# Performance work log

Hardware: AMD Instinct MI355X
Metric: run time of the kernel (lower is better)

Reference implementation:

```python
import jax, jax.numpy as jnp
import numpy as np

R = 5            # num_relations
NEG_SLOPE = 0.2
N1 = 30000       # layer0 target count
N2 = 15000       # layer1 target count


def brgcn_conv(x_src, x_tgt, edge_index, edge_type, Wj, Wi, att_j, att_i,
               Wq, Wk, Wv, sw, sb, Wrel, heads, outc):
    """One BRGCNConv layer: per-relation GAT edge softmax + bilevel relation attention."""
    N = x_tgt.shape[0]
    hc = heads * outc
    hj = (x_src @ Wj).reshape(-1, heads, outc)   # [Ns,H,C]
    hi = (x_tgt @ Wi).reshape(-1, heads, outc)   # [N,H,C]
    src, tgt = edge_index[0], edge_index[1]
    xj = hj[src]                                  # [E,H,C]
    xi = hi[tgt]                                  # [E,H,C]
    # relation-specific attention logits per edge
    aj = jnp.sum(att_j[edge_type] * xj, axis=-1)  # [E,H]
    ai = jnp.sum(att_i[edge_type] * xi, axis=-1)  # [E,H]
    alpha = jax.nn.leaky_relu(aj + ai, NEG_SLOPE)
    # edge softmax grouped by (target node, relation) == per-relation propagate
    seg = tgt * R + edge_type                     # [E]
    nseg = N * R
    amax = jax.ops.segment_max(alpha, seg, num_segments=nseg)
    amax = jnp.where(jnp.isfinite(amax), amax, 0.0)
    ex = jnp.exp(alpha - amax[seg])
    den = jax.ops.segment_sum(ex, seg, num_segments=nseg)
    w = ex / jnp.maximum(den[seg], 1e-16)         # [E,H]
    msg = (w[:, :, None] * xj).reshape(-1, hc)    # [E,H*C]
    z = jax.ops.segment_sum(msg, seg, num_segments=nseg)
    z = z.reshape(N, R, hc).transpose(1, 0, 2)    # [R,N,H*C]; zero rows where no edges
    # per-relation Q/K/V
    q = jnp.einsum('rnd,rde->rne', z, Wq).reshape(R, N, heads, outc)
    k = jnp.einsum('rnd,rde->rne', z, Wk).reshape(R, N, heads, outc)
    v = jnp.einsum('rnd,rde->rne', z, Wv).reshape(R, N, heads, outc)
    # bilevel relation attention: psi[r,s,n,h] = <q_r, k_s>
    psi = jnp.einsum('rnhc,snhc->rsnh', q, k)
    mask = (psi == 0) & (jnp.sum(psi, axis=1, keepdims=True) != 0)
    prob = jax.nn.softmax(jnp.where(mask, -jnp.inf, psi), axis=1)
    delta = jnp.einsum('rsnh,snhc->rnhc', prob, v).reshape(R, N, hc)
    out = jnp.einsum('rnd,r->nd', delta, Wrel[:, 0])
    # single node type -> node_self[0] applied to every target node
    return out + x_tgt @ sw + sb


def setup_inputs() -> dict:
    key = jax.random.key(0)
    ks = jax.random.split(key, 32)
    H0, C0, H1, C1 = 4, 64, 1, 40
    IN, HC0 = 128, H0 * C0
    NG, N0 = 200000, 100000
    E0, E1 = 300000, 150000
    f = lambda k, s: jax.random.normal(k, s, dtype=jnp.float32) * 0.05
    return dict(
        n_id=jax.random.randint(ks[1], (N0,), 0, NG),
        local_node_idx=jax.random.randint(ks[2], (NG,), 0, NG),
        node_type=jnp.zeros((NG,), dtype=jnp.int32),
        edge_index0=jax.random.randint(ks[3], (2, E0), 0, N1),
        edge_type0=jax.random.randint(ks[4], (E0,), 0, R),
        edge_index1=jax.random.randint(ks[5], (2, E1), 0, N2),
        edge_type1=jax.random.randint(ks[6], (E1,), 0, R),
        emb=f(ks[0], (NG, IN)),
        Wj0=f(ks[7], (IN, HC0)), Wi0=f(ks[8], (IN, HC0)),
        att_j0=f(ks[9], (R, H0, C0)), att_i0=f(ks[10], (R, H0, C0)),
        Wq0=f(ks[11], (R, HC0, HC0)), Wk0=f(ks[12], (R, HC0, HC0)), Wv0=f(ks[13], (R, HC0, HC0)),
        sw0=f(ks[14], (IN, HC0)), sb0=f(ks[15], (HC0,)), Wrel0=f(ks[16], (R, 1)),
        Wj1=f(ks[17], (HC0, C1)), Wi1=f(ks[18], (HC0, C1)),
        att_j1=f(ks[19], (R, H1, C1)), att_i1=f(ks[20], (R, H1, C1)),
        Wq1=f(ks[21], (R, C1, C1)), Wk1=f(ks[22], (R, C1, C1)), Wv1=f(ks[23], (R, C1, C1)),
        sw1=f(ks[24], (HC0, C1)), sb1=f(ks[25], (C1,)), Wrel1=f(ks[26], (R, 1)),
    )


def reference(n_id, local_node_idx, node_type, edge_index0, edge_type0,
              edge_index1, edge_type1, emb,
              Wj0, Wi0, att_j0, att_i0, Wq0, Wk0, Wv0, sw0, sb0, Wrel0,
              Wj1, Wi1, att_j1, att_i1, Wq1, Wk1, Wv1, sw1, sb1, Wrel1):
    # group_input: single node type, all features from the embedding table
    x = emb[local_node_idx[n_id]]
    x1 = brgcn_conv(x, x[:N1], edge_index0, edge_type0, Wj0, Wi0, att_j0, att_i0,
                    Wq0, Wk0, Wv0, sw0, sb0, Wrel0, heads=4, outc=64)
    x1 = jax.nn.relu(x1)  # dropout p=0 in eval
    x2 = brgcn_conv(x1, x1[:N2], edge_index1, edge_type1, Wj1, Wi1, att_j1, att_i1,
                    Wq1, Wk1, Wv1, sw1, sb1, Wrel1, heads=1, outc=40)
    return jax.nn.log_softmax(x2, axis=-1)
```

## Files before the change

kernel.cpp:

```cpp
#include <hip/hip_runtime.h>
#include <hip/hip_bf16.h>

#define DI __device__ __forceinline__

DI float b2f(unsigned short u) {
    union { unsigned int i; float f; } x; x.i = ((unsigned int)u) << 16; return x.f;
}
DI unsigned short f2b(float f) {
    union { float f; unsigned int i; } x; x.f = f;
    unsigned int r = x.i + 0x7fff + ((x.i >> 16) & 1);
    return (unsigned short)(r >> 16);
}
DI float ldin(const void* p, long i, int f32) {
    return f32 ? ((const float*)p)[i] : b2f(((const unsigned short*)p)[i]);
}
DI void stval(float* p, float v) { *p = v; }
DI void stval(unsigned short* p, float v) { *p = f2b(v); }

static constexpr int N1 = 30000, N2 = 15000, R = 5;
static constexpr int IN = 128, HC0 = 256, C1 = 40;
static constexpr float NEGBIG = -1e30f;
static constexpr int LDK = 64;

typedef short bf16x8 __attribute__((ext_vector_type(8)));
typedef float f32x4 __attribute__((ext_vector_type(4)));

__global__ void detect_k(const void* emb, int* flag)
{
    int lane = threadIdx.x;
    int bad = 0;
    for (int j = 0; j < 4; ++j) {
        float f = b2f(((const unsigned short*)emb)[lane * 4 + j]);
        if (!(fabsf(f) < 1e8f)) bad = 1;
    }
    unsigned long long anybad = __ballot(bad != 0);
    if (lane == 0) *flag = (anybad != 0ull) ? 1 : 0;
}

struct PrepJobs {
    const void* src[12];
    unsigned short* dst[12];
    int K[12];
    int N[12];
    int per[12];
};
__global__ __launch_bounds__(256) void prep_all_k(
    PrepJobs J,
    const void* aj0, const void* ai0, const void* aj1, const void* ai1,
    unsigned short* A0j, unsigned short* A0i, unsigned short* A1j, unsigned short* A1i,
    int* __restrict__ cnt, int cntn,
    const int* __restrict__ dflag)
{
    const int f32 = *dflag;
    const int y = blockIdx.y;
    long t = (long)blockIdx.x * 256 + threadIdx.x;
    if (y < 12) {
        if (t >= J.per[y]) return;
        const int K = J.K[y], N = J.N[y];
        long kn = (long)K * N;
        long b = t / kn, rem = t % kn;
        long k = rem / N, n = rem % N;
        J.dst[y][(b * N + n) * K + k] = f2b(ldin(J.src[y], t, f32));
    } else {
        if (t < 20 * 256) {
            int j = (int)(t >> 8), k = (int)(t & 255);
            int h = j & 3, r = j >> 2;
            bool on = (k >> 6) == h;
            A0j[t] = f2b(on ? ldin(aj0, r * 256 + k, f32) : 0.f);
            A0i[t] = f2b(on ? ldin(ai0, r * 256 + k, f32) : 0.f);
        }
        if (t < 5 * 40) {
            A1j[t] = f2b(ldin(aj1, t, f32));
            A1i[t] = f2b(ldin(ai1, t, f32));
        }
        if (t < cntn) cnt[t] = 0;
    }
}

__global__ __launch_bounds__(256) void gather_k(
    const int* __restrict__ n_id, const int* __restrict__ lidx,
    const void* __restrict__ emb, unsigned short* __restrict__ x, int rows,
    const int* __restrict__ dflag)
{
    const int f32 = *dflag;
    long t = (long)blockIdx.x * 256 + threadIdx.x;
    long n = t >> 7, d = t & 127;
    if (n >= rows) return;
    long row = lidx[n_id[n]];
    x[n * IN + d] = f2b(ldin(emb, row * IN + d, f32));
}


DI void gload_lds16(const unsigned short* src, unsigned short* dst)
{
    __builtin_amdgcn_global_load_lds(
        (const __attribute__((address_space(1))) unsigned int*)src,
        (__attribute__((address_space(3))) unsigned int*)dst, 16, 0, 0);
}

DI void stage_fast(const unsigned short* __restrict__ G, int K,
                   unsigned short* S, int wave, int lane)
{
    const int p = lane >> 3;
    const int scol = ((lane & 7) ^ p) * 8;
#pragma unroll
    for (int t = 0; t < 4; ++t) {
        int row = t * 32 + wave * 8 + p;
        gload_lds16(G + (long)row * K + scol, S + (t * 32 + wave * 8) * LDK);
    }
}
DI void stage_fast8(const unsigned short* __restrict__ G, int K,
                    unsigned short* S, int wave, int lane)
{
    const int p = lane >> 3;
    const int scol = ((lane & 7) ^ p) * 8;
#pragma unroll
    for (int t = 0; t < 2; ++t) {
        int row = wave * 16 + t * 8 + p;
        gload_lds16(G + (long)row * K + scol, S + (wave * 16 + t * 8) * LDK);
    }
}
DI void stage_slow(const unsigned short* __restrict__ G, int rows, int K,
                   int r0, int k0, unsigned short* S, int tid)
{
    const int sr = tid >> 1, sq = (tid & 1) * 32;
    const int sx = sr & 7;
    unsigned short* drow = S + sr * LDK;
    const unsigned short* g = G + (long)(r0 + sr) * K + k0 + sq;
    const bool rowok = (r0 + sr) < rows;
    const int s0 = sq >> 3;
    if (rowok && (k0 + sq + 32) <= K) {
        const uint4* gv = (const uint4*)g;
        uint4 a = gv[0], b = gv[1], c = gv[2], d = gv[3];
        *(uint4*)(drow + (((s0 + 0) ^ sx) << 3)) = a;
        *(uint4*)(drow + (((s0 + 1) ^ sx) << 3)) = b;
        *(uint4*)(drow + (((s0 + 2) ^ sx) << 3)) = c;
        *(uint4*)(drow + (((s0 + 3) ^ sx) << 3)) = d;
    } else if (!rowok) {
        uint4 zz = {0u, 0u, 0u, 0u};
        *(uint4*)(drow + (((s0 + 0) ^ sx) << 3)) = zz;
        *(uint4*)(drow + (((s0 + 1) ^ sx) << 3)) = zz;
        *(uint4*)(drow + (((s0 + 2) ^ sx) << 3)) = zz;
        *(uint4*)(drow + (((s0 + 3) ^ sx) << 3)) = zz;
    } else {
#pragma unroll 8
        for (int j = 0; j < 32; ++j) {
            int col = sq + j;
            int k = k0 + col;
            int widx = (((col >> 3) ^ sx) << 3) | (col & 7);
            drow[widx] = (k < K) ? g[j] : (unsigned short)0;
        }
    }
}

template <int KK>
__global__ __launch_bounds__(512) void gemm_ares4_k(
    const unsigned short* __restrict__ Ab,
    const unsigned short* B0, const unsigned short* B1, const unsigned short* B2,
    unsigned short* C0, unsigned short* C1, unsigned short* C2,
    const void* bias0, const void* bias1, const void* bias2,
    const int* __restrict__ dflag,
    int M, long sA, long sB, long sC)
{
    __shared__ unsigned short As[128 * KK];
    __shared__ unsigned short Bs[128 * LDK];
    const int f32 = *dflag;
    const int tid = threadIdx.x;
    const int lane = tid & 63, wave = tid >> 6;
    const int b = blockIdx.z;
    const int n0 = blockIdx.x * 128, m0 = blockIdx.y * 128;
    const int wm = (wave & 1) * 64, wn = (wave >> 1) * 32;
    const int row16 = lane & 15, quad = lane >> 4;

    {
        const unsigned short* Gb = Ab + (long)b * sA + (long)m0 * KK;
        if (KK == 256) {
            const int lrow = lane >> 5, slin = lane & 31;
#pragma unroll
            for (int t = 0; t < 8; ++t) {
                int rbase = wave * 16 + t * 2;
                int row = rbase + lrow;
                gload_lds16(Gb + (long)row * 256 + ((slin ^ (row & 7)) << 3),
                            As + rbase * 256);
            }
        } else {
            const int lrow = lane >> 4, slin = lane & 15;
#pragma unroll
            for (int t = 0; t < 4; ++t) {
                int rbase = wave * 16 + t * 4;
                int row = rbase + lrow;
                gload_lds16(Gb + (long)row * 128 + ((slin ^ (row & 7)) << 3),
                            As + rbase * 128);
            }
        }
    }

#pragma unroll 1
    for (int sel = 0; sel < 3; ++sel) {
        const unsigned short* Bt = (sel == 0 ? B0 : sel == 1 ? B1 : B2)
                                   + (long)b * sB + (long)n0 * KK;
        unsigned short* C = (sel == 0 ? C0 : sel == 1 ? C1 : C2) + (long)b * sC;
        const void* bias = sel == 0 ? bias0 : sel == 1 ? bias1 : bias2;
        f32x4 acc[4][2];
#pragma unroll
        for (int i = 0; i < 4; ++i)
#pragma unroll
            for (int j = 0; j < 2; ++j) acc[i][j] = {0.f, 0.f, 0.f, 0.f};

        for (int k0 = 0; k0 < KK; k0 += 64) {
            stage_fast8(Bt + k0, KK, Bs, wave, lane);
            __syncthreads();
#pragma unroll
            for (int ks = 0; ks < 64; ks += 32) {
                const int kk = k0 + ks;
                const int saw = ((((kk >> 3) + quad) ^ (row16 & 7)) << 3);
                const int sbw = ((((ks >> 3) + quad) ^ (row16 & 7)) << 3);
                bf16x8 af[4], bfr[2];
#pragma unroll
                for (int i = 0; i < 4; ++i)
                    af[i] = *(const bf16x8*)(As + (wm + i * 16 + row16) * KK + saw);
#pragma unroll
                for (int j = 0; j < 2; ++j)
                    bfr[j] = *(const bf16x8*)(Bs + (wn + j * 16 + row16) * LDK + sbw);
#pragma unroll
                for (int i = 0; i < 4; ++i)
#pragma unroll
                    for (int j = 0; j < 2; ++j)
                        acc[i][j] = __builtin_amdgcn_mfma_f32_16x16x32_bf16(
                            af[i], bfr[j], acc[i][j], 0, 0, 0);
            }
            __syncthreads();
        }
#pragma unroll
        for (int i = 0; i < 4; ++i) {
#pragma unroll
            for (int reg = 0; reg < 4; ++reg) {
                const int gr = m0 + wm + i * 16 + quad * 4 + reg;
                if (gr >= M) continue;
#pragma unroll
                for (int j = 0; j < 2; ++j) {
                    const int gc = n0 + wn + j * 16 + row16;
                    float v = acc[i][j][reg];
                    if (bias) v += ldin(bias, gc, f32);
                    C[(long)gr * 256 + gc] = f2b(v);
                }
            }
        }
    }
}

template <typename OT>
DI void gemm_mfma_body(
    const unsigned short* __restrict__ A, const unsigned short* __restrict__ Bt,
    OT* __restrict__ C, const void* __restrict__ bias, int f32,
    int M, int N, int K, unsigned short* As, unsigned short* Bs)
{
    const int tid = threadIdx.x;
    const int m0 = blockIdx.y * 128, n0 = blockIdx.x * 128;
    const int lane = tid & 63, wave = tid >> 6;
    const int wm = (wave & 1) * 64, wn = (wave >> 1) * 64;
    const int row16 = lane & 15, quad = lane >> 4;
    const bool kfull = (K & 63) == 0;
    const bool fastA = kfull && (m0 + 128 <= M);
    const bool fastB = kfull && (n0 + 128 <= N);
    f32x4 acc[4][4];
#pragma unroll
    for (int i = 0; i < 4; ++i)
#pragma unroll
        for (int j = 0; j < 4; ++j) acc[i][j] = {0.f, 0.f, 0.f, 0.f};

    for (int k0 = 0; k0 < K; k0 += 64) {
        if (fastA) stage_fast(A + (long)m0 * K + k0, K, As, wave, lane);
        else       stage_slow(A, M, K, m0, k0, As, tid);
        if (fastB) stage_fast(Bt + (long)n0 * K + k0, K, Bs, wave, lane);
        else       stage_slow(Bt, N, K, n0, k0, Bs, tid);
        __syncthreads();
#pragma unroll
        for (int ks = 0; ks < 64; ks += 32) {
            const int sw = (((quad + (ks >> 3)) ^ (row16 & 7)) << 3);
            bf16x8 af[4], bfr[4];
#pragma unroll
            for (int i = 0; i < 4; ++i)
                af[i] = *(const bf16x8*)(As + (wm + i * 16 + row16) * LDK + sw);
#pragma unroll
            for (int j = 0; j < 4; ++j)
                bfr[j] = *(const bf16x8*)(Bs + (wn + j * 16 + row16) * LDK + sw);
#pragma unroll
            for (int i = 0; i < 4; ++i)
#pragma unroll
                for (int j = 0; j < 4; ++j)
                    acc[i][j] = __builtin_amdgcn_mfma_f32_16x16x32_bf16(
                        af[i], bfr[j], acc[i][j], 0, 0, 0);
        }
        __syncthreads();
    }
#pragma unroll
    for (int i = 0; i < 4; ++i) {
#pragma unroll
        for (int reg = 0; reg < 4; ++reg) {
            const int gr = m0 + wm + i * 16 + quad * 4 + reg;
            if (gr >= M) continue;
#pragma unroll
            for (int j = 0; j < 4; ++j) {
                const int gc = n0 + wn + j * 16 + row16;
                if (gc >= N) continue;
                float v = acc[i][j][reg];
                if (bias) v += ldin(bias, gc, f32);
                stval(&C[(long)gr * N + gc], v);
            }
        }
    }
}

template <typename OT>
__global__ __launch_bounds__(256) void gemm_mfma3_k(
    const unsigned short* A0, const unsigned short* A1, const unsigned short* A2,
    const unsigned short* Bt0, const unsigned short* Bt1, const unsigned short* Bt2,
    OT* C0, OT* C1, OT* C2,
    const void* bias0, const void* bias1, const void* bias2,
    const int* __restrict__ dflag,
    int M, int N, int K, long sA, long sB, long sC, int nbatch)
{
    __shared__ unsigned short As[128 * LDK];
    __shared__ unsigned short Bs[128 * LDK];
    const int f32 = *dflag;
    const int sel = blockIdx.z / nbatch, b = blockIdx.z % nbatch;
    const unsigned short* A  = (sel == 0 ? A0 : sel == 1 ? A1 : A2) + (long)b * sA;
    const unsigned short* Bt = (sel == 0 ? Bt0 : sel == 1 ? Bt1 : Bt2) + (long)b * sB;
    OT* C = (sel == 0 ? C0 : sel == 1 ? C1 : C2) + (long)b * sC;
    const void* bias = sel == 0 ? bias0 : sel == 1 ? bias1 : bias2;
    gemm_mfma_body<OT>(A, Bt, C, bias, f32, M, N, K, As, Bs);
}

__global__ __launch_bounds__(256) void hist_k(const int* __restrict__ ei, int E, int* __restrict__ cnt)
{
    int e = blockIdx.x * 256 + threadIdx.x;
    if (e < E) atomicAdd(&cnt[ei[E + e]], 1);
}
__global__ __launch_bounds__(256) void scan1_k(
    const int* __restrict__ cnt, int* __restrict__ off, int* __restrict__ bsum, int n)
{
    __shared__ int buf[256];
    int i = blockIdx.x * 256 + threadIdx.x;
    int v = (i < n) ? cnt[i] : 0;
    buf[threadIdx.x] = v;
    __syncthreads();
#pragma unroll
    for (int s = 1; s < 256; s <<= 1) {
        int t = (threadIdx.x >= s) ? buf[threadIdx.x - s] : 0;
        __syncthreads();
        buf[threadIdx.x] += t;
        __syncthreads();
    }
    if (i < n) off[i] = buf[threadIdx.x] - v;
    if (threadIdx.x == 255) bsum[blockIdx.x] = buf[255];
}
__global__ void scan2_k(int* __restrict__ bsum, int nb, int* __restrict__ total_dst)
{
    __shared__ int buf[256];
    int v = (threadIdx.x < nb) ? bsum[threadIdx.x] : 0;
    buf[threadIdx.x] = v;
    __syncthreads();
#pragma unroll
    for (int s = 1; s < 256; s <<= 1) {
        int t = (threadIdx.x >= s) ? buf[threadIdx.x - s] : 0;
        __syncthreads();
        buf[threadIdx.x] += t;
        __syncthreads();
    }
    if (threadIdx.x < nb) bsum[threadIdx.x] = buf[threadIdx.x] - v;
    if (threadIdx.x == 255) *total_dst = buf[255];
}
__global__ __launch_bounds__(256) void scan3_k(
    int* __restrict__ off, int* __restrict__ cursor, const int* __restrict__ bsum,
    int* __restrict__ cnt, int n)
{
    int i = blockIdx.x * 256 + threadIdx.x;
    if (i < n) {
        int v = off[i] + bsum[blockIdx.x];
        off[i] = v;
        cursor[i] = v;
        cnt[i] = 0;
    }
}

__global__ __launch_bounds__(256) void scatter0_k(
    const int* __restrict__ ei, const int* __restrict__ et, int E,
    int* __restrict__ cursor,
    const float* __restrict__ ajn, const float* __restrict__ ain,
    int* __restrict__ src_s, int* __restrict__ rt_s, float* __restrict__ w4_s)
{
    int e = blockIdx.x * 256 + threadIdx.x;
    if (e >= E) return;
    int src = ei[e], tgt = ei[E + e], r = et[e];
    int p = atomicAdd(&cursor[tgt], 1);
    src_s[p] = src; rt_s[p] = r;
    float4 a = *(const float4*)(ajn + (long)src * 20 + r * 4);
    float4 b = *(const float4*)(ain + (long)tgt * 20 + r * 4);
    float4 w;
    float s0 = a.x + b.x, s1 = a.y + b.y, s2 = a.z + b.z, s3 = a.w + b.w;
    s0 = s0 > 0.f ? s0 : 0.2f * s0;  s1 = s1 > 0.f ? s1 : 0.2f * s1;
    s2 = s2 > 0.f ? s2 : 0.2f * s2;  s3 = s3 > 0.f ? s3 : 0.2f * s3;
    w.x = expf(fminf(s0, 60.f)); w.y = expf(fminf(s1, 60.f));
    w.z = expf(fminf(s2, 60.f)); w.w = expf(fminf(s3, 60.f));
    *(float4*)(w4_s + (long)p * 4) = w;
}
__global__ __launch_bounds__(256) void scatter1_k(
    const int* __restrict__ ei, const int* __restrict__ et, int E,
    int* __restrict__ cursor,
    const float* __restrict__ ajn, const float* __restrict__ ain,
    int* __restrict__ src_s, int* __restrict__ rt_s, float* __restrict__ w_s)
{
    int e = blockIdx.x * 256 + threadIdx.x;
    if (e >= E) return;
    int src = ei[e], tgt = ei[E + e], r = et[e];
    int p = atomicAdd(&cursor[tgt], 1);
    src_s[p] = src; rt_s[p] = r;
    float s = ajn[(long)src * 5 + r] + ain[(long)tgt * 5 + r];
    s = s > 0.f ? s : 0.2f * s;
    w_s[p] = expf(fminf(s, 60.f));
}

__global__ __launch_bounds__(256) void aggregate0_k(
    const int* __restrict__ src_s, const int* __restrict__ rt_s,
    const float* __restrict__ w4_s, const int* __restrict__ off,
    const unsigned short* __restrict__ hj,
    unsigned short* __restrict__ z, int Nn)
{
    int tgt = (int)((blockIdx.x * 256u + threadIdx.x) >> 6);
    int lane = threadIdx.x & 63;
    if (tgt >= Nn) return;
    int dd = lane * 4, h = lane >> 4;
    float acc[5][4] = {};
    float den[5] = {};
    int s = off[tgt], epd = off[tgt + 1];
    for (int i = s; i < epd; ++i) {
        int src = src_s[i];
        int r_e = rt_s[i];
        float wgt = w4_s[(long)i * 4 + h];
        ushort4 xj = *(const ushort4*)(hj + (long)src * 256 + dd);
        float x0 = b2f(xj.x), x1 = b2f(xj.y), x2 = b2f(xj.z), x3 = b2f(xj.w);
#pragma unroll
        for (int r = 0; r < 5; ++r) {
            float ws = (r == r_e) ? wgt : 0.f;
            den[r] += ws;
            acc[r][0] += ws * x0; acc[r][1] += ws * x1;
            acc[r][2] += ws * x2; acc[r][3] += ws * x3;
        }
    }
#pragma unroll
    for (int r = 0; r < 5; ++r) {
        float inv = 1.f / fmaxf(den[r], 1e-16f);
        ushort4 o;
        o.x = f2b(acc[r][0] * inv); o.y = f2b(acc[r][1] * inv);
        o.z = f2b(acc[r][2] * inv); o.w = f2b(acc[r][3] * inv);
        *(ushort4*)(z + ((long)r * Nn + tgt) * 256 + dd) = o;
    }
}

__global__ __launch_bounds__(256) void aggregate1_k(
    const int* __restrict__ src_s, const int* __restrict__ rt_s,
    const float* __restrict__ w_s, const int* __restrict__ off,
    const unsigned short* __restrict__ hj,
    unsigned short* __restrict__ z, int Nn)
{
    int tgt = (int)((blockIdx.x * 256u + threadIdx.x) >> 6);
    int lane = threadIdx.x & 63;
    if (tgt >= Nn) return;
    bool act = lane < 40;
    float acc[5] = {};
    float den[5] = {};
    int s = off[tgt], epd = off[tgt + 1];
    for (int i = s; i < epd; ++i) {
        int src = src_s[i];
        int r_e = rt_s[i];
        float wgt = w_s[i];
        float xj = act ? b2f(hj[(long)src * 40 + lane]) : 0.f;
#pragma unroll
        for (int r = 0; r < 5; ++r) {
            float ws = (r == r_e) ? wgt : 0.f;
            den[r] += ws;
            acc[r] += ws * xj;
        }
    }
    if (act) {
#pragma unroll
        for (int r = 0; r < 5; ++r) {
            float inv = 1.f / fmaxf(den[r], 1e-16f);
            z[((long)r * Nn + tgt) * 40 + lane] = f2b(acc[r] * inv);
        }
    }
}

__global__ __launch_bounds__(256) void fused_attn0_k(
    const unsigned short* __restrict__ qb, const unsigned short* __restrict__ kb,
    const unsigned short* __restrict__ vb, const void* __restrict__ wrel,
    unsigned short* __restrict__ x1, int n0, int nloc, int chq,
    const int* __restrict__ dflag)
{
    const int f32 = *dflag;
    int nl = (int)((blockIdx.x * 256u + threadIdx.x) >> 6);
    int lane = threadIdx.x & 63;
    if (nl >= nloc) return;
    int n = n0 + nl;
    int dd = lane * 4;
    float qf[5][4], kf[5][4];
#pragma unroll
    for (int r = 0; r < 5; ++r) {
        ushort4 qv = *(const ushort4*)(qb + ((long)r * chq + nl) * 256 + dd);
        ushort4 kv = *(const ushort4*)(kb + ((long)r * chq + nl) * 256 + dd);
        qf[r][0] = b2f(qv.x); qf[r][1] = b2f(qv.y); qf[r][2] = b2f(qv.z); qf[r][3] = b2f(qv.w);
        kf[r][0] = b2f(kv.x); kf[r][1] = b2f(kv.y); kf[r][2] = b2f(kv.z); kf[r][3] = b2f(kv.w);
    }
    float psi[5][5];
#pragma unroll
    for (int r = 0; r < 5; ++r)
#pragma unroll
        for (int s = 0; s < 5; ++s) {
            float p = qf[r][0] * kf[s][0] + qf[r][1] * kf[s][1] +
                      qf[r][2] * kf[s][2] + qf[r][3] * kf[s][3];
            p += __shfl_xor(p, 1, 64); p += __shfl_xor(p, 2, 64);
            p += __shfl_xor(p, 4, 64); p += __shfl_xor(p, 8, 64);
            psi[r][s] = p;
        }
    float pw[5] = {0.f, 0.f, 0.f, 0.f, 0.f};
#pragma unroll
    for (int r = 0; r < 5; ++r) {
        float rowsum = psi[r][0] + psi[r][1] + psi[r][2] + psi[r][3] + psi[r][4];
        float vals[5], m = NEGBIG;
#pragma unroll
        for (int s = 0; s < 5; ++s) {
            float v = (psi[r][s] == 0.f && rowsum != 0.f) ? NEGBIG : psi[r][s];
            vals[s] = v; m = fmaxf(m, v);
        }
        float es[5], sum = 0.f;
#pragma unroll
        for (int s = 0; s < 5; ++s) { es[s] = expf(vals[s] - m); sum += es[s]; }
        float wr = ldin(wrel, r, f32) / sum;
#pragma unroll
        for (int s = 0; s < 5; ++s) pw[s] += wr * es[s];
    }
    float acc[4] = {0.f, 0.f, 0.f, 0.f};
#pragma unroll
    for (int s = 0; s < 5; ++s) {
        ushort4 vv = *(const ushort4*)(vb + ((long)s * chq + nl) * 256 + dd);
        acc[0] += pw[s] * b2f(vv.x); acc[1] += pw[s] * b2f(vv.y);
        acc[2] += pw[s] * b2f(vv.z); acc[3] += pw[s] * b2f(vv.w);
    }
    ushort4* xp = (ushort4*)(x1 + (long)n * 256 + dd);
    ushort4 sv = *xp;
    sv.x = f2b(fmaxf(b2f(sv.x) + acc[0], 0.f));
    sv.y = f2b(fmaxf(b2f(sv.y) + acc[1], 0.f));
    sv.z = f2b(fmaxf(b2f(sv.z) + acc[2], 0.f));
    sv.w = f2b(fmaxf(b2f(sv.w) + acc[3], 0.f));
    *xp = sv;
}

__global__ __launch_bounds__(256) void fused_attn1_k(
    const unsigned short* __restrict__ qb, const unsigned short* __restrict__ kb,
    const unsigned short* __restrict__ vb, const void* __restrict__ wrel,
    const unsigned short* __restrict__ self1, void* __restrict__ out, int N,
    const int* __restrict__ dflag)
{
    const int f32 = *dflag;
    int n = (int)((blockIdx.x * 256u + threadIdx.x) >> 6);
    int lane = threadIdx.x & 63;
    if (n >= N) return;
    bool act = lane < 40;
    float qf[5], kf[5];
#pragma unroll
    for (int r = 0; r < 5; ++r) {
        long o = ((long)r * N + n) * 40 + lane;
        qf[r] = act ? b2f(qb[o]) : 0.f;
        kf[r] = act ? b2f(kb[o]) : 0.f;
    }
    float psi[5][5];
#pragma unroll
    for (int r = 0; r < 5; ++r)
#pragma unroll
        for (int s = 0; s < 5; ++s) {
            float p = qf[r] * kf[s];
            p += __shfl_xor(p, 1, 64);  p += __shfl_xor(p, 2, 64);
            p += __shfl_xor(p, 4, 64);  p += __shfl_xor(p, 8, 64);
            p += __shfl_xor(p, 16, 64); p += __shfl_xor(p, 32, 64);
            psi[r][s] = p;
        }
    float pw[5] = {0.f, 0.f, 0.f, 0.f, 0.f};
#pragma unroll
    for (int r = 0; r < 5; ++r) {
        float rowsum = psi[r][0] + psi[r][1] + psi[r][2] + psi[r][3] + psi[r][4];
        float vals[5], m = NEGBIG;
#pragma unroll
        for (int s = 0; s < 5; ++s) {
            float v = (psi[r][s] == 0.f && rowsum != 0.f) ? NEGBIG : psi[r][s];
            vals[s] = v; m = fmaxf(m, v);
        }
        float es[5], sum = 0.f;
#pragma unroll
        for (int s = 0; s < 5; ++s) { es[s] = expf(vals[s] - m); sum += es[s]; }
        float wr = ldin(wrel, r, f32) / sum;
#pragma unroll
        for (int s = 0; s < 5; ++s) pw[s] += wr * es[s];
    }
    float val = NEGBIG;
    if (act) {
        float acc = 0.f;
#pragma unroll
        for (int s = 0; s < 5; ++s) acc += pw[s] * b2f(vb[((long)s * N + n) * 40 + lane]);
        val = b2f(self1[(long)n * 40 + lane]) + acc;
    }
    float m = val;
#pragma unroll
    for (int msk = 1; msk < 64; msk <<= 1) m = fmaxf(m, __shfl_xor(m, msk, 64));
    float e = act ? expf(val - m) : 0.f;
#pragma unroll
    for (int msk = 1; msk < 64; msk <<= 1) e += __shfl_xor(e, msk, 64);
    if (act) {
        float r = val - m - logf(e);
        long oidx = (long)n * 40 + lane;
        if (f32) ((float*)out)[oidx] = r;
        else     ((unsigned short*)out)[oidx] = f2b(r);
    }
}

extern "C" void kernel_launch(void* const* d_in, const int* in_sizes, int n_in,
                              void* d_out, int out_size, void* d_ws, size_t ws_size,
                              hipStream_t stream)
{
    const int* n_id = (const int*)d_in[0];
    const int* lidx = (const int*)d_in[1];
    const int* ei0  = (const int*)d_in[3];
    const int* et0  = (const int*)d_in[4];
    const int* ei1  = (const int*)d_in[5];
    const int* et1  = (const int*)d_in[6];
    const void* emb = d_in[7];
    const void* Wj0 = d_in[8];  const void* Wi0 = d_in[9];
    const void* aj0 = d_in[10]; const void* ai0 = d_in[11];
    const void* Wq0 = d_in[12]; const void* Wk0 = d_in[13]; const void* Wv0 = d_in[14];
    const void* sw0 = d_in[15]; const void* sb0 = d_in[16]; const void* Wr0 = d_in[17];
    const void* Wj1 = d_in[18]; const void* Wi1 = d_in[19];
    const void* aj1 = d_in[20]; const void* ai1 = d_in[21];
    const void* Wq1 = d_in[22]; const void* Wk1 = d_in[23]; const void* Wv1 = d_in[24];
    const void* sw1 = d_in[25]; const void* sb1 = d_in[26]; const void* Wr1 = d_in[27];
    const int E0 = in_sizes[4], E1 = in_sizes[6];

    auto al = [](size_t b) { return (b + 255) & ~(size_t)255; };

    const size_t P_total =
        al((size_t)R * N1 * HC0 * 2) +
        al((size_t)N1 * HC0 * 2) +
        2 * al((size_t)N1 * 20 * 4) +
        3 * al((size_t)(N1 + 1) * 4) +
        al(256 * 4) +
        2 * al((size_t)E0 * 4) +
        al((size_t)E0 * 16) +
        3 * al((size_t)HC0 * IN * 2) +
        3 * al((size_t)R * HC0 * HC0 * 2) +
        3 * al((size_t)C1 * HC0 * 2) +
        3 * al((size_t)R * C1 * C1 * 2) +
        2 * al(20 * 256 * 2) + 2 * al(5 * 40 * 2) +
        al(256);

    int CH = N1;
    {
        auto need = [&](int ch) {
            return 3 * al((size_t)R * ch * HC0 * 2) + P_total + (16u << 20);
        };
        if (need(CH) > ws_size) CH = 15000;
        if (need(CH) > ws_size) CH = 7500;
    }
    const size_t QB = al((size_t)R * CH * HC0 * 2);

    char* w = (char*)d_ws;
    unsigned short* qc = (unsigned short*)(w);
    unsigned short* kc = (unsigned short*)(w + QB);
    unsigned short* vc = (unsigned short*)(w + 2 * QB);
    unsigned short* x30k = (unsigned short*)(w);
    unsigned short* hj0  = (unsigned short*)(w + al((size_t)N1 * IN * 2));
    unsigned short* hi0  = (unsigned short*)((char*)hj0 + al((size_t)N1 * HC0 * 2));
    size_t o1 = 0;
    auto take1 = [&](size_t b) { char* p = w + o1; o1 += (b + 255) & ~(size_t)255; return p; };
    unsigned short* hj1   = (unsigned short*)take1((size_t)N2 * C1 * 2);
    unsigned short* hi1   = (unsigned short*)take1((size_t)N2 * C1 * 2);
    unsigned short* self1 = (unsigned short*)take1((size_t)N2 * C1 * 2);
    float* ajn1 = (float*)take1((size_t)N2 * R * 4);
    float* ain1 = (float*)take1((size_t)N2 * R * 4);
    unsigned short* z1  = (unsigned short*)take1((size_t)R * N2 * C1 * 2);
    unsigned short* q1b = (unsigned short*)take1((size_t)R * N2 * C1 * 2);
    unsigned short* k1b = (unsigned short*)take1((size_t)R * N2 * C1 * 2);
    unsigned short* v1b = (unsigned short*)take1((size_t)R * N2 * C1 * 2);
    size_t o = 3 * QB;
    auto take = [&](size_t b) { char* p = w + o; o += (b + 255) & ~(size_t)255; return p; };
    unsigned short* z0 = (unsigned short*)take((size_t)R * N1 * HC0 * 2);
    unsigned short* x1 = (unsigned short*)take((size_t)N1 * HC0 * 2);
    float* ajn0 = (float*)take((size_t)N1 * 20 * 4);
    float* ain0 = (float*)take((size_t)N1 * 20 * 4);
    int* cnt    = (int*)take((size_t)(N1 + 1) * 4);
    int* off    = (int*)take((size_t)(N1 + 1) * 4);
    int* cursor = (int*)take((size_t)(N1 + 1) * 4);
    int* bsum   = (int*)take(256 * 4);
    int* src_s  = (int*)take((size_t)E0 * 4);
    int* rt_s   = (int*)take((size_t)E0 * 4);
    float* w4_s = (float*)take((size_t)E0 * 16);
    unsigned short* wjt0 = (unsigned short*)take((size_t)HC0 * IN * 2);
    unsigned short* wit0 = (unsigned short*)take((size_t)HC0 * IN * 2);
    unsigned short* swt0 = (unsigned short*)take((size_t)HC0 * IN * 2);
    unsigned short* wqt0 = (unsigned short*)take((size_t)R * HC0 * HC0 * 2);
    unsigned short* wkt0 = (unsigned short*)take((size_t)R * HC0 * HC0 * 2);
    unsigned short* wvt0 = (unsigned short*)take((size_t)R * HC0 * HC0 * 2);
    unsigned short* wjt1 = (unsigned short*)take((size_t)C1 * HC0 * 2);
    unsigned short* wit1 = (unsigned short*)take((size_t)C1 * HC0 * 2);
    unsigned short* swt1 = (unsigned short*)take((size_t)C1 * HC0 * 2);
    unsigned short* wqt1 = (unsigned short*)take((size_t)R * C1 * C1 * 2);
    unsigned short* wkt1 = (unsigned short*)take((size_t)R * C1 * C1 * 2);
    unsigned short* wvt1 = (unsigned short*)take((size_t)R * C1 * C1 * 2);
    unsigned short* atA0j = (unsigned short*)take(20 * 256 * 2);
    unsigned short* atA0i = (unsigned short*)take(20 * 256 * 2);
    unsigned short* atA1j = (unsigned short*)take(5 * 40 * 2);
    unsigned short* atA1i = (unsigned short*)take(5 * 40 * 2);
    int* dflag = (int*)take(256);

    detect_k<<<1, 64, 0, stream>>>(emb, dflag);

    {
        PrepJobs J;
        const void* srcs[12] = {Wj0, Wi0, sw0, Wq0, Wk0, Wv0, Wj1, Wi1, sw1, Wq1, Wk1, Wv1};
        unsigned short* dsts[12] = {wjt0, wit0, swt0, wqt0, wkt0, wvt0,
                                    wjt1, wit1, swt1, wqt1, wkt1, wvt1};
        int Ks[12] = {IN, IN, IN, HC0, HC0, HC0, HC0, HC0, HC0, C1, C1, C1};
        int Ns[12] = {HC0, HC0, HC0, HC0, HC0, HC0, C1, C1, C1, C1, C1, C1};
        int pers[12] = {IN * HC0, IN * HC0, IN * HC0,
                        R * HC0 * HC0, R * HC0 * HC0, R * HC0 * HC0,
                        HC0 * C1, HC0 * C1, HC0 * C1,
                        R * C1 * C1, R * C1 * C1, R * C1 * C1};
        for (int i = 0; i < 12; ++i) {
            J.src[i] = srcs[i]; J.dst[i] = dsts[i];
            J.K[i] = Ks[i]; J.N[i] = Ns[i]; J.per[i] = pers[i];
        }
        int xb = (R * HC0 * HC0 + 255) / 256;
        prep_all_k<<<dim3((unsigned)xb, 13), 256, 0, stream>>>(
            J, aj0, ai0, aj1, ai1, atA0j, atA0i, atA1j, atA1i, cnt, N1 + 1, dflag);
    }

    gather_k<<<(int)(((long)N1 * IN + 255) / 256), 256, 0, stream>>>(n_id, lidx, emb, x30k, N1, dflag);
    gemm_ares4_k<128><<<dim3(2, (N1 + 127) / 128, 1), 512, 0, stream>>>(
        x30k, wjt0, wit0, swt0, hj0, hi0, x1, nullptr, nullptr, sb0,
        dflag, N1, 0, 0, 0);
    gemm_mfma3_k<float><<<dim3(1, (N1 + 127) / 128, 2), 256, 0, stream>>>(
        hj0, hi0, hi0, atA0j, atA0i, atA0i, ajn0, ain0, ain0, nullptr, nullptr, nullptr,
        dflag, N1, 20, HC0, 0, 0, 0, 1);

    hist_k<<<(E0 + 255) / 256, 256, 0, stream>>>(ei0, E0, cnt);
    {
        int nb = (N1 + 255) / 256;
        scan1_k<<<nb, 256, 0, stream>>>(cnt, off, bsum, N1);
        scan2_k<<<1, 256, 0, stream>>>(bsum, nb, off + N1);
        scan3_k<<<nb, 256, 0, stream>>>(off, cursor, bsum, cnt, N1);
    }
    scatter0_k<<<(E0 + 255) / 256, 256, 0, stream>>>(ei0, et0, E0, cursor, ajn0, ain0, src_s, rt_s, w4_s);
    aggregate0_k<<<(N1 + 3) / 4, 256, 0, stream>>>(src_s, rt_s, w4_s, off, hj0, z0, N1);

    {
        const int nch = N1 / CH;
        for (int c = 0; c < nch; ++c) {
            const unsigned short* zc = z0 + (long)c * CH * HC0;
            gemm_ares4_k<256><<<dim3(2, (CH + 127) / 128, R), 512, 0, stream>>>(
                zc, wqt0, wkt0, wvt0, qc, kc, vc, nullptr, nullptr, nullptr,
                dflag, CH, (long)N1 * HC0, (long)HC0 * HC0, (long)CH * HC0);
            fused_attn0_k<<<(CH + 3) / 4, 256, 0, stream>>>(qc, kc, vc, Wr0, x1, c * CH, CH, CH, dflag);
        }
    }

    gemm_mfma3_k<unsigned short><<<dim3(1, (N2 + 127) / 128, 3), 256, 0, stream>>>(
        x1, x1, x1, wjt1, wit1, swt1, hj1, hi1, self1, nullptr, nullptr, sb1,
        dflag, N2, C1, HC0, 0, 0, 0, 1);
    gemm_mfma3_k<float><<<dim3(1, (N2 + 127) / 128, 2), 256, 0, stream>>>(
        hj1, hi1, hi1, atA1j, atA1i, atA1i, ajn1, ain1, ain1, nullptr, nullptr, nullptr,
        dflag, N2, 5, C1, 0, 0, 0, 1);

    hist_k<<<(E1 + 255) / 256, 256, 0, stream>>>(ei1, E1, cnt);
    {
        int nb = (N2 + 255) / 256;
        scan1_k<<<nb, 256, 0, stream>>>(cnt, off, bsum, N2);
        scan2_k<<<1, 256, 0, stream>>>(bsum, nb, off + N2);
        scan3_k<<<nb, 256, 0, stream>>>(off, cursor, bsum, cnt, N2);
    }
    scatter1_k<<<(E1 + 255) / 256, 256, 0, stream>>>(ei1, et1, E1, cursor, ajn1, ain1, src_s, rt_s, w4_s);
    aggregate1_k<<<(N2 + 3) / 4, 256, 0, stream>>>(src_s, rt_s, w4_s, off, hj1, z1, N2);

    {
        long sA = (long)N2 * C1, sB = (long)C1 * C1, sC = (long)N2 * C1;
        gemm_mfma3_k<unsigned short><<<dim3(1, (N2 + 127) / 128, 3 * R), 256, 0, stream>>>(
            z1, z1, z1, wqt1, wkt1, wvt1, q1b, k1b, v1b, nullptr, nullptr, nullptr,
            dflag, N2, C1, C1, sA, sB, sC, R);
    }
    fused_attn1_k<<<(N2 + 3) / 4, 256, 0, stream>>>(q1b, k1b, v1b, Wr1, self1, d_out, N2, dflag);
}
```

Baseline: 603.4 us.

## Fuse V projection with relation-attention weighting into one GEMM epilogue

The layer-0 V projection is removed from the per-chunk Q/K/V GEMM, and the attention kernel now writes only the per-node, per-relation, per-head probability weights to a small buffer. A new GEMM kernel computes V for every relation, rounds it to bf16, scales it by those weights, accumulates across relations in registers, and adds the result into x1 with ReLU. This avoids writing and reading the V tensor through global memory. In exchange the new kernel loops over the five relations serially inside each block, and staging A for each relation may reduce parallelism.

```diff
diff --git a/kernel.cpp b/kernel.cpp
--- a/kernel.cpp
+++ b/kernel.cpp
@@ -118,6 +118,30 @@
     for (int t = 0; t < 2; ++t) {
         int row = wave * 16 + t * 8 + p;
         gload_lds16(G + (long)row * K + scol, S + (wave * 16 + t * 8) * LDK);
+    }
+}
+template <int KK>
+DI void stageA8(const unsigned short* __restrict__ Gb, unsigned short* As,
+                int wave, int lane)
+{
+    if (KK == 256) {
+        const int lrow = lane >> 5, slin = lane & 31;
+#pragma unroll
+        for (int t = 0; t < 8; ++t) {
+            int rbase = wave * 16 + t * 2;
+            int row = rbase + lrow;
+            gload_lds16(Gb + (long)row * 256 + ((slin ^ (row & 7)) << 3),
+                        As + rbase * 256);
+        }
+    } else {
+        const int lrow = lane >> 4, slin = lane & 15;
+#pragma unroll
+        for (int t = 0; t < 4; ++t) {
+            int rbase = wave * 16 + t * 4;
+            int row = rbase + lrow;
+            gload_lds16(Gb + (long)row * 128 + ((slin ^ (row & 7)) << 3),
+                        As + rbase * 128);
+        }
     }
 }
 DI void stage_slow(const unsigned short* __restrict__ G, int rows, int K,
@@ -160,7 +184,7 @@
     unsigned short* C0, unsigned short* C1, unsigned short* C2,
     const void* bias0, const void* bias1, const void* bias2,
     const int* __restrict__ dflag,
-    int M, long sA, long sB, long sC)
+    int M, long sA, long sB, long sC, int nsel)
 {
     __shared__ unsigned short As[128 * KK];
     __shared__ unsigned short Bs[128 * LDK];
@@ -172,31 +196,10 @@
     const int wm = (wave & 1) * 64, wn = (wave >> 1) * 32;
     const int row16 = lane & 15, quad = lane >> 4;
 
-    {
-        const unsigned short* Gb = Ab + (long)b * sA + (long)m0 * KK;
-        if (KK == 256) {
-            const int lrow = lane >> 5, slin = lane & 31;
-#pragma unroll
-            for (int t = 0; t < 8; ++t) {
-                int rbase = wave * 16 + t * 2;
-                int row = rbase + lrow;
-                gload_lds16(Gb + (long)row * 256 + ((slin ^ (row & 7)) << 3),
-                            As + rbase * 256);
-            }
-        } else {
-            const int lrow = lane >> 4, slin = lane & 15;
-#pragma unroll
-            for (int t = 0; t < 4; ++t) {
-                int rbase = wave * 16 + t * 4;
-                int row = rbase + lrow;
-                gload_lds16(Gb + (long)row * 128 + ((slin ^ (row & 7)) << 3),
-                            As + rbase * 128);
-            }
-        }
-    }
+    stageA8<KK>(Ab + (long)b * sA + (long)m0 * KK, As, wave, lane);
 
 #pragma unroll 1
-    for (int sel = 0; sel < 3; ++sel) {
+    for (int sel = 0; sel < nsel; ++sel) {
         const unsigned short* Bt = (sel == 0 ? B0 : sel == 1 ? B1 : B2)
                                    + (long)b * sB + (long)n0 * KK;
         unsigned short* C = (sel == 0 ? C0 : sel == 1 ? C1 : C2) + (long)b * sC;
@@ -244,6 +247,94 @@
                     if (bias) v += ldin(bias, gc, f32);
                     C[(long)gr * 256 + gc] = f2b(v);
                 }
+            }
+        }
+    }
+}
+
+__global__ __launch_bounds__(512) void gemm_wv_k(
+    const unsigned short* __restrict__ z0,
+    const unsigned short* __restrict__ Bt,
+    const float* __restrict__ pw,
+    unsigned short* __restrict__ x1,
+    int M)
+{
+    __shared__ unsigned short As[128 * 256];
+    __shared__ unsigned short Bs[128 * LDK];
+    const int tid = threadIdx.x;
+    const int lane = tid & 63, wave = tid >> 6;
+    const int n0 = blockIdx.x * 128, m0 = blockIdx.y * 128;
+    const int wm = (wave & 1) * 64, wn = (wave >> 1) * 32;
+    const int row16 = lane & 15, quad = lane >> 4;
+
+    f32x4 acct[4][2];
+#pragma unroll
+    for (int i = 0; i < 4; ++i)
+#pragma unroll
+        for (int j = 0; j < 2; ++j) acct[i][j] = {0.f, 0.f, 0.f, 0.f};
+
+#pragma unroll 1
+    for (int r = 0; r < R; ++r) {
+        stageA8<256>(z0 + ((long)r * M + m0) * 256, As, wave, lane);
+        const unsigned short* Btr = Bt + ((long)r * 256 + n0) * 256;
+        f32x4 vac[4][2];
+#pragma unroll
+        for (int i = 0; i < 4; ++i)
+#pragma unroll
+            for (int j = 0; j < 2; ++j) vac[i][j] = {0.f, 0.f, 0.f, 0.f};
+
+        for (int k0 = 0; k0 < 256; k0 += 64) {
+            stage_fast8(Btr + k0, 256, Bs, wave, lane);
+            __syncthreads();
+#pragma unroll
+            for (int ks = 0; ks < 64; ks += 32) {
+                const int kk = k0 + ks;
+                const int saw = ((((kk >> 3) + quad) ^ (row16 & 7)) << 3);
+                const int sbw = ((((ks >> 3) + quad) ^ (row16 & 7)) << 3);
+                bf16x8 af[4], bfr[2];
+#pragma unroll
+                for (int i = 0; i < 4; ++i)
+                    af[i] = *(const bf16x8*)(As + (wm + i * 16 + row16) * 256 + saw);
+#pragma unroll
+                for (int j = 0; j < 2; ++j)
+                    bfr[j] = *(const bf16x8*)(Bs + (wn + j * 16 + row16) * LDK + sbw);
+#pragma unroll
+                for (int i = 0; i < 4; ++i)
+#pragma unroll
+                    for (int j = 0; j < 2; ++j)
+                        vac[i][j] = __builtin_amdgcn_mfma_f32_16x16x32_bf16(
+                            af[i], bfr[j], vac[i][j], 0, 0, 0);
+            }
+            __syncthreads();
+        }
+#pragma unroll
+        for (int i = 0; i < 4; ++i) {
+#pragma unroll
+            for (int reg = 0; reg < 4; ++reg) {
+                const int gr = m0 + wm + i * 16 + quad * 4 + reg;
+                if (gr >= M) continue;
+#pragma unroll
+                for (int j = 0; j < 2; ++j) {
+                    const int gc = n0 + wn + j * 16 + row16;
+                    const int h = gc >> 6;
+                    float pv = pw[(long)gr * 20 + r * 4 + h];
+                    acct[i][j][reg] += pv * b2f(f2b(vac[i][j][reg]));
+                }
+            }
+        }
+    }
+#pragma unroll
+    for (int i = 0; i < 4; ++i) {
+#pragma unroll
+        for (int reg = 0; reg < 4; ++reg) {
+            const int gr = m0 + wm + i * 16 + quad * 4 + reg;
+            if (gr >= M) continue;
+#pragma unroll
+            for (int j = 0; j < 2; ++j) {
+                const int gc = n0 + wn + j * 16 + row16;
+                long idx = (long)gr * 256 + gc;
+                float s = b2f(x1[idx]) + acct[i][j][reg];
+                x1[idx] = f2b(fmaxf(s, 0.f));
             }
         }
     }
@@ -492,10 +583,10 @@
     }
 }
 
-__global__ __launch_bounds__(256) void fused_attn0_k(
+__global__ __launch_bounds__(256) void attn_pw_k(
     const unsigned short* __restrict__ qb, const unsigned short* __restrict__ kb,
-    const unsigned short* __restrict__ vb, const void* __restrict__ wrel,
-    unsigned short* __restrict__ x1, int n0, int nloc, int chq,
+    const void* __restrict__ wrel,
+    float* __restrict__ pw_g, int n0, int nloc, int chq,
     const int* __restrict__ dflag)
 {
     const int f32 = *dflag;
@@ -503,7 +594,7 @@
     int lane = threadIdx.x & 63;
     if (nl >= nloc) return;
     int n = n0 + nl;
-    int dd = lane * 4;
+    int dd = lane * 4, h = lane >> 4;
     float qf[5][4], kf[5][4];
 #pragma unroll
     for (int r = 0; r < 5; ++r) {
@@ -540,20 +631,11 @@
 #pragma unroll
         for (int s = 0; s < 5; ++s) pw[s] += wr * es[s];
     }
-    float acc[4] = {0.f, 0.f, 0.f, 0.f};
-#pragma unroll
-    for (int s = 0; s < 5; ++s) {
-        ushort4 vv = *(const ushort4*)(vb + ((long)s * chq + nl) * 256 + dd);
-        acc[0] += pw[s] * b2f(vv.x); acc[1] += pw[s] * b2f(vv.y);
-        acc[2] += pw[s] * b2f(vv.z); acc[3] += pw[s] * b2f(vv.w);
-    }
-    ushort4* xp = (ushort4*)(x1 + (long)n * 256 + dd);
-    ushort4 sv = *xp;
-    sv.x = f2b(fmaxf(b2f(sv.x) + acc[0], 0.f));
-    sv.y = f2b(fmaxf(b2f(sv.y) + acc[1], 0.f));
-    sv.z = f2b(fmaxf(b2f(sv.z) + acc[2], 0.f));
-    sv.w = f2b(fmaxf(b2f(sv.w) + acc[3], 0.f));
-    *xp = sv;
+    if ((lane & 15) == 0) {
+#pragma unroll
+        for (int s = 0; s < 5; ++s)
+            pw_g[(long)n * 20 + s * 4 + h] = pw[s];
+    }
 }
 
 __global__ __launch_bounds__(256) void fused_attn1_k(
@@ -649,6 +731,7 @@
     const size_t P_total =
         al((size_t)R * N1 * HC0 * 2) +
         al((size_t)N1 * HC0 * 2) +
+        al((size_t)N1 * 20 * 4) +
         2 * al((size_t)N1 * 20 * 4) +
         3 * al((size_t)(N1 + 1) * 4) +
         al(256 * 4) +
@@ -674,7 +757,6 @@
     char* w = (char*)d_ws;
     unsigned short* qc = (unsigned short*)(w);
     unsigned short* kc = (unsigned short*)(w + QB);
-    unsigned short* vc = (unsigned short*)(w + 2 * QB);
     unsigned short* x30k = (unsigned short*)(w);
     unsigned short* hj0  = (unsigned short*)(w + al((size_t)N1 * IN * 2));
     unsigned short* hi0  = (unsigned short*)((char*)hj0 + al((size_t)N1 * HC0 * 2));
@@ -693,6 +775,7 @@
     auto take = [&](size_t b) { char* p = w + o; o += (b + 255) & ~(size_t)255; return p; };
     unsigned short* z0 = (unsigned short*)take((size_t)R * N1 * HC0 * 2);
     unsigned short* x1 = (unsigned short*)take((size_t)N1 * HC0 * 2);
+    float* pwb  = (float*)take((size_t)N1 * 20 * 4);
     float* ajn0 = (float*)take((size_t)N1 * 20 * 4);
     float* ain0 = (float*)take((size_t)N1 * 20 * 4);
     int* cnt    = (int*)take((size_t)(N1 + 1) * 4);
@@ -745,7 +828,7 @@
     gather_k<<<(int)(((long)N1 * IN + 255) / 256), 256, 0, stream>>>(n_id, lidx, emb, x30k, N1, dflag);
     gemm_ares4_k<128><<<dim3(2, (N1 + 127) / 128, 1), 512, 0, stream>>>(
         x30k, wjt0, wit0, swt0, hj0, hi0, x1, nullptr, nullptr, sb0,
-        dflag, N1, 0, 0, 0);
+        dflag, N1, 0, 0, 0, 3);
     gemm_mfma3_k<float><<<dim3(1, (N1 + 127) / 128, 2), 256, 0, stream>>>(
         hj0, hi0, hi0, atA0j, atA0i, atA0i, ajn0, ain0, ain0, nullptr, nullptr, nullptr,
         dflag, N1, 20, HC0, 0, 0, 0, 1);
@@ -765,10 +848,12 @@
         for (int c = 0; c < nch; ++c) {
             const unsigned short* zc = z0 + (long)c * CH * HC0;
             gemm_ares4_k<256><<<dim3(2, (CH + 127) / 128, R), 512, 0, stream>>>(
-                zc, wqt0, wkt0, wvt0, qc, kc, vc, nullptr, nullptr, nullptr,
-                dflag, CH, (long)N1 * HC0, (long)HC0 * HC0, (long)CH * HC0);
-            fused_attn0_k<<<(CH + 3) / 4, 256, 0, stream>>>(qc, kc, vc, Wr0, x1, c * CH, CH, CH, dflag);
-        }
+                zc, wqt0, wkt0, nullptr, qc, kc, nullptr, nullptr, nullptr, nullptr,
+                dflag, CH, (long)N1 * HC0, (long)HC0 * HC0, (long)CH * HC0, 2);
+            attn_pw_k<<<(CH + 3) / 4, 256, 0, stream>>>(qc, kc, Wr0, pwb, c * CH, CH, CH, dflag);
+        }
+        gemm_wv_k<<<dim3(2, (N1 + 127) / 128), 512, 0, stream>>>(
+            z0, wvt0, pwb, x1, N1);
     }
 
     gemm_mfma3_k<unsigned short><<<dim3(1, (N2 + 127) / 128, 3), 256, 0, stream>>>(
```

After: 703.8 us. 1.17x slower.

## Fuse three-output GEMM into single K loop with shared A tile

Applied to the files above, without the earlier changes.

Restructures the multi-output GEMM so one K-loop stages a 64-wide slice of A plus all three B slices per iteration and accumulates all three outputs at once, instead of holding the whole A tile in LDS and looping over the three weight matrices serially. This reduces LDS footprint (A no longer stored for full K), cuts the number of barriers and K-loop passes, and lets each A fragment feed three MFMA groups. In exchange it triples live accumulators per thread, raising register pressure, and the launch bound now requests 4 blocks per CU, which may force spills.

```diff
diff --git a/kernel.cpp b/kernel.cpp
--- a/kernel.cpp
+++ b/kernel.cpp
@@ -154,7 +154,7 @@
 }
 
 template <int KK>
-__global__ __launch_bounds__(512) void gemm_ares4_k(
+__global__ __launch_bounds__(512, 4) void gemm_ares7_k(
     const unsigned short* __restrict__ Ab,
     const unsigned short* B0, const unsigned short* B1, const unsigned short* B2,
     unsigned short* C0, unsigned short* C1, unsigned short* C2,
@@ -162,8 +162,10 @@
     const int* __restrict__ dflag,
     int M, long sA, long sB, long sC)
 {
-    __shared__ unsigned short As[128 * KK];
-    __shared__ unsigned short Bs[128 * LDK];
+    __shared__ unsigned short AsC[128 * LDK];
+    __shared__ unsigned short Bs0[128 * LDK];
+    __shared__ unsigned short Bs1[128 * LDK];
+    __shared__ unsigned short Bs2[128 * LDK];
     const int f32 = *dflag;
     const int tid = threadIdx.x;
     const int lane = tid & 63, wave = tid >> 6;
@@ -172,78 +174,91 @@
     const int wm = (wave & 1) * 64, wn = (wave >> 1) * 32;
     const int row16 = lane & 15, quad = lane >> 4;
 
-    {
-        const unsigned short* Gb = Ab + (long)b * sA + (long)m0 * KK;
-        if (KK == 256) {
-            const int lrow = lane >> 5, slin = lane & 31;
-#pragma unroll
-            for (int t = 0; t < 8; ++t) {
-                int rbase = wave * 16 + t * 2;
-                int row = rbase + lrow;
-                gload_lds16(Gb + (long)row * 256 + ((slin ^ (row & 7)) << 3),
-                            As + rbase * 256);
+    const unsigned short* Abase = Ab + (long)b * sA + (long)m0 * KK;
+    const unsigned short* Bb0 = B0 + (long)b * sB + (long)n0 * KK;
+    const unsigned short* Bb1 = B1 + (long)b * sB + (long)n0 * KK;
+    const unsigned short* Bb2 = B2 + (long)b * sB + (long)n0 * KK;
+
+    f32x4 acc0[4][2], acc1[4][2], acc2[4][2];
+#pragma unroll
+    for (int i = 0; i < 4; ++i)
+#pragma unroll
+        for (int j = 0; j < 2; ++j) {
+            acc0[i][j] = {0.f, 0.f, 0.f, 0.f};
+            acc1[i][j] = {0.f, 0.f, 0.f, 0.f};
+            acc2[i][j] = {0.f, 0.f, 0.f, 0.f};
+        }
+
+    for (int k0 = 0; k0 < KK; k0 += 64) {
+        stage_fast8(Abase + k0, KK, AsC, wave, lane);
+        stage_fast8(Bb0 + k0, KK, Bs0, wave, lane);
+        stage_fast8(Bb1 + k0, KK, Bs1, wave, lane);
+        stage_fast8(Bb2 + k0, KK, Bs2, wave, lane);
+        __syncthreads();
+#pragma unroll
+        for (int ks = 0; ks < 64; ks += 32) {
+            const int sw = ((((ks >> 3) + quad) ^ (row16 & 7)) << 3);
+            bf16x8 af[4];
+#pragma unroll
+            for (int i = 0; i < 4; ++i)
+                af[i] = *(const bf16x8*)(AsC + (wm + i * 16 + row16) * LDK + sw);
+            {
+                bf16x8 bfr[2];
+#pragma unroll
+                for (int j = 0; j < 2; ++j)
+                    bfr[j] = *(const bf16x8*)(Bs0 + (wn + j * 16 + row16) * LDK + sw);
+#pragma unroll
+                for (int i = 0; i < 4; ++i)
+#pragma unroll
+                    for (int j = 0; j < 2; ++j)
+                        acc0[i][j] = __builtin_amdgcn_mfma_f32_16x16x32_bf16(
+                            af[i], bfr[j], acc0[i][j], 0, 0, 0);
             }
-        } else {
-            const int lrow = lane >> 4, slin = lane & 15;
-#pragma unroll
-            for (int t = 0; t < 4; ++t) {
-                int rbase = wave * 16 + t * 4;
-                int row = rbase + lrow;
-                gload_lds16(Gb + (long)row * 128 + ((slin ^ (row & 7)) << 3),
-                            As + rbase * 128);
+            {
+                bf16x8 bfr[2];
+#pragma unroll
+                for (int j = 0; j < 2; ++j)
+                    bfr[j] = *(const bf16x8*)(Bs1 + (wn + j * 16 + row16) * LDK + sw);
+#pragma unroll
+                for (int i = 0; i < 4; ++i)
+#pragma unroll
+                    for (int j = 0; j < 2; ++j)
+                        acc1[i][j] = __builtin_amdgcn_mfma_f32_16x16x32_bf16(
+                            af[i], bfr[j], acc1[i][j], 0, 0, 0);
             }
-        }
-    }
-
-#pragma unroll 1
-    for (int sel = 0; sel < 3; ++sel) {
-        const unsigned short* Bt = (sel == 0 ? B0 : sel == 1 ? B1 : B2)
-                                   + (long)b * sB + (long)n0 * KK;
-        unsigned short* C = (sel == 0 ? C0 : sel == 1 ? C1 : C2) + (long)b * sC;
-        const void* bias = sel == 0 ? bias0 : sel == 1 ? bias1 : bias2;
-        f32x4 acc[4][2];
-#pragma unroll
-        for (int i = 0; i < 4; ++i)
-#pragma unroll
-            for (int j = 0; j < 2; ++j) acc[i][j] = {0.f, 0.f, 0.f, 0.f};
-
-        for (int k0 = 0; k0 < KK; k0 += 64) {
-            stage_fast8(Bt + k0, KK, Bs, wave, lane);
-            __syncthreads();
-#pragma unroll
-            for (int ks = 0; ks < 64; ks += 32) {
-                const int kk = k0 + ks;
-                const int saw = ((((kk >> 3) + quad) ^ (row16 & 7)) << 3);
-                const int sbw = ((((ks >> 3) + quad) ^ (row16 & 7)) << 3);
-                bf16x8 af[4], bfr[2];
+            {
+                bf16x8 bfr[2];
+#pragma unroll
+                for (int j = 0; j < 2; ++j)
+                    bfr[j] = *(const bf16x8*)(Bs2 + (wn + j * 16 + row16) * LDK + sw);
 #pragma unroll
                 for (int i = 0; i < 4; ++i)
-                    af[i] = *(const bf16x8*)(As + (wm + i * 16 + row16) * KK + saw);
-#pragma unroll
-                for (int j = 0; j < 2; ++j)
-                    bfr[j] = *(const bf16x8*)(Bs + (wn + j * 16 + row16) * LDK + sbw);
-#pragma unroll
-                for (int i = 0; i < 4; ++i)
 #pragma unroll
                     for (int j = 0; j < 2; ++j)
-                        acc[i][j] = __builtin_amdgcn_mfma_f32_16x16x32_bf16(
-                            af[i], bfr[j], acc[i][j], 0, 0, 0);
+                        acc2[i][j] = __builtin_amdgcn_mfma_f32_16x16x32_bf16(
+                            af[i], bfr[j], acc2[i][j], 0, 0, 0);
             }
-            __syncthreads();
-        }
-#pragma unroll
-        for (int i = 0; i < 4; ++i) {
-#pragma unroll
-            for (int reg = 0; reg < 4; ++reg) {
-                const int gr = m0 + wm + i * 16 + quad * 4 + reg;
-                if (gr >= M) continue;
-#pragma unroll
-                for (int j = 0; j < 2; ++j) {
-                    const int gc = n0 + wn + j * 16 + row16;
-                    float v = acc[i][j][reg];
-                    if (bias) v += ldin(bias, gc, f32);
-                    C[(long)gr * 256 + gc] = f2b(v);
-                }
+        }
+        __syncthreads();
+    }
+#pragma unroll
+    for (int i = 0; i < 4; ++i) {
+#pragma unroll
+        for (int reg = 0; reg < 4; ++reg) {
+            const int gr = m0 + wm + i * 16 + quad * 4 + reg;
+            if (gr >= M) continue;
+#pragma unroll
+            for (int j = 0; j < 2; ++j) {
+                const int gc = n0 + wn + j * 16 + row16;
+                float v0 = acc0[i][j][reg];
+                if (bias0) v0 += ldin(bias0, gc, f32);
+                C0[(long)b * sC + (long)gr * 256 + gc] = f2b(v0);
+                float v1 = acc1[i][j][reg];
+                if (bias1) v1 += ldin(bias1, gc, f32);
+                C1[(long)b * sC + (long)gr * 256 + gc] = f2b(v1);
+                float v2 = acc2[i][j][reg];
+                if (bias2) v2 += ldin(bias2, gc, f32);
+                C2[(long)b * sC + (long)gr * 256 + gc] = f2b(v2);
             }
         }
     }
@@ -743,7 +758,7 @@
     }
 
     gather_k<<<(int)(((long)N1 * IN + 255) / 256), 256, 0, stream>>>(n_id, lidx, emb, x30k, N1, dflag);
-    gemm_ares4_k<128><<<dim3(2, (N1 + 127) / 128, 1), 512, 0, stream>>>(
+    gemm_ares7_k<128><<<dim3(2, (N1 + 127) / 128, 1), 512, 0, stream>>>(
         x30k, wjt0, wit0, swt0, hj0, hi0, x1, nullptr, nullptr, sb0,
         dflag, N1, 0, 0, 0);
     gemm_mfma3_k<float><<<dim3(1, (N1 + 127) / 128, 2), 256, 0, stream>>>(
@@ -764,7 +779,7 @@
         const int nch = N1 / CH;
         for (int c = 0; c < nch; ++c) {
             const unsigned short* zc = z0 + (long)c * CH * HC0;
-            gemm_ares4_k<256><<<dim3(2, (CH + 127) / 128, R), 512, 0, stream>>>(
+            gemm_ares7_k<256><<<dim3(2, (CH + 127) / 128, R), 512, 0, stream>>>(
                 zc, wqt0, wkt0, wvt0, qc, kc, vc, nullptr, nullptr, nullptr,
                 dflag, CH, (long)N1 * HC0, (long)HC0 * HC0, (long)CH * HC0);
             fused_attn0_k<<<(CH + 3) / 4, 256, 0, stream>>>(qc, kc, vc, Wr0, x1, c * CH, CH, CH, dflag);
```

Result: slower. 695.8 us (+15.3%).
